# Kernel tuning notes

Measured on AMD Instinct MI355X. Metric: run time of the kernel, lower is better.

The kernel has to match this reference:

```python
import jax, jax.numpy as jnp
import numpy as np

B, L, D = 16, 1024, 768

def setup_inputs() -> dict:
    key = jax.random.key(0)
    ks = jax.random.split(key, 6)
    s = 1.0 / np.sqrt(D)  # torch Linear default init scale
    return {
        "h": jax.random.normal(ks[0], (B, L, D), dtype=jnp.float32),
        "q": jax.random.normal(ks[1], (B, L, D), dtype=jnp.float32),
        "w1_w": jax.random.uniform(ks[2], (L, D), jnp.float32, -s, s),
        "w1_b": jax.random.uniform(ks[3], (L,), jnp.float32, -s, s),
        "w2_w": jax.random.uniform(ks[4], (L, D), jnp.float32, -s, s),
        "w2_b": jax.random.uniform(ks[5], (L,), jnp.float32, -s, s),
    }

def reference(h, q, w1_w, w1_b, w2_w, w2_b):
    # w1h: [B, L, l], w2q: [B, L, l] -> permuted [B, l, L]
    w1h = jnp.einsum('bsd,ld->bsl', h, w1_w) + w1_b
    w2q = jnp.einsum('btd,ld->btl', q, w2_w) + w2_b
    w3hq = jnp.einsum('bsd,btd->bst', h, q)           # [B, L, L]
    a = w1h + jnp.swapaxes(w2q, 1, 2) + w3hq          # [B, L, L]
    p = jax.nn.softmax(a, axis=2)
    c = jnp.einsum('bst,btd->bsd', p, q)              # [B, L, D]
    m = jnp.max(a, axis=2)                            # [B, L]
    p2 = jax.nn.softmax(m, axis=1)                    # [B, L]
    qc = h * p2[:, :, None]                           # [B, L, D]
    return jnp.concatenate([h, c, h * c, qc * c], axis=2)  # [B, L, 4D]
```

## Files before the change

### kernel.cpp

```cpp
#include <hip/hip_runtime.h>
#include <stdint.h>

#define B_  16
#define L_  1024
#define D_  768
#define K1_ 1536

typedef unsigned short u16;
typedef __attribute__((ext_vector_type(4))) float f32x4;
typedef __attribute__((ext_vector_type(8))) _Float16 f16x8;

__device__ __forceinline__ u16 f2h(float x){
    return __builtin_bit_cast(u16, (_Float16)x);
}

__device__ __forceinline__ void gload_lds16(const void* g, void* l){
    __builtin_amdgcn_global_load_lds((const __attribute__((address_space(1))) void*)g,
                                     (__attribute__((address_space(3))) void*)l, 16, 0, 0);
}

__global__ __launch_bounds__(256) void prep(const float* __restrict__ h, const float* __restrict__ q,
    const float* __restrict__ w1w, const float* __restrict__ w2w,
    u16* __restrict__ hH, u16* __restrict__ wH, u16* __restrict__ qH,
    u16* __restrict__ w1h, u16* __restrict__ qT, int b0, int nb)
{
    __shared__ float tile[32][33];
    int bb = blockIdx.z, bg = b0 + bb;
    int t0 = blockIdx.x * 32, d0 = blockIdx.y * 32;
    int tid = threadIdx.x;
    int r  = tid >> 3;
    int c4 = (tid & 7) * 4;
    int t = t0 + r, d = d0 + c4;
    size_t goff = (size_t)t * D_ + d;

    float4 qv  = *(const float4*)(q   + (size_t)bg * L_ * D_ + goff);
    float4 hv  = *(const float4*)(h   + (size_t)bg * L_ * D_ + goff);
    float4 w2v = *(const float4*)(w2w + goff);

    tile[r][c4 + 0] = qv.x; tile[r][c4 + 1] = qv.y;
    tile[r][c4 + 2] = qv.z; tile[r][c4 + 3] = qv.w;

    size_t o = ((size_t)bb * L_ + t) * D_ + d;
    ushort4 a;
    a.x = f2h(hv.x); a.y = f2h(hv.y); a.z = f2h(hv.z); a.w = f2h(hv.w);
    *(ushort4*)(hH + o) = a;
    a.x = f2h(hv.x + w2v.x); a.y = f2h(hv.y + w2v.y);
    a.z = f2h(hv.z + w2v.z); a.w = f2h(hv.w + w2v.w);
    *(ushort4*)(wH + o) = a;
    a.x = f2h(qv.x); a.y = f2h(qv.y); a.z = f2h(qv.z); a.w = f2h(qv.w);
    *(ushort4*)(qH + o) = a;
    if (bb == 0){
        float4 w1v = *(const float4*)(w1w + goff);
        a.x = f2h(w1v.x); a.y = f2h(w1v.y); a.z = f2h(w1v.z); a.w = f2h(w1v.w);
        *(ushort4*)(w1h + goff) = a;
    }
    __syncthreads();
    int dr = tid >> 3;
    int tc = (tid & 7) * 4;
    ushort4 b;
    b.x = f2h(tile[tc + 0][dr]); b.y = f2h(tile[tc + 1][dr]);
    b.z = f2h(tile[tc + 2][dr]); b.w = f2h(tile[tc + 3][dr]);
    *(ushort4*)(qT + (size_t)bb * D_ * L_ + (size_t)(d0 + dr) * L_ + t0 + tc) = b;
}

__global__ __launch_bounds__(512) void gemm1(
    const u16* __restrict__ hH, const u16* __restrict__ wH,
    const u16* __restrict__ qH, const u16* __restrict__ w1h,
    const float* __restrict__ w1b, const float* __restrict__ w2b,
    u16* __restrict__ pT, float* __restrict__ mT, float* __restrict__ sT)
{
    __shared__ u16 ldsA[2][256 * 64];
    __shared__ u16 ldsB[2][256 * 64];
    int nwg = gridDim.x;
    int o = blockIdx.x;
    int wg = (o & 7) * (nwg >> 3) + (o >> 3);
    int bb = wg >> 4;
    int tl = wg & 15;
    int smb = tl >> 2, tnb = tl & 3;
    int s0 = smb * 256, t0 = tnb * 256;
    int tid = threadIdx.x;
    int lane = tid & 63, wid = tid >> 6;
    int wm2 = wid >> 2, wn2 = wid & 3;
    int l15 = lane & 15, l4 = lane >> 4;

    const u16* hHb = hH + (size_t)bb * L_ * D_;
    const u16* wHb = wH + (size_t)bb * L_ * D_;
    const u16* qHb = qH + (size_t)bb * L_ * D_;

    f32x4 acc[8][4];
    #pragma unroll
    for (int m = 0; m < 8; m++)
        #pragma unroll
        for (int n = 0; n < 4; n++)
            acc[m][n] = (f32x4){0.f, 0.f, 0.f, 0.f};

    auto stage = [&](int t){
        int kb = t * 64;
        bool inH = (kb < D_);
        const u16* As = inH ? hHb : wHb;
        const u16* Bs = inH ? w1h : qHb;
        int koff = inH ? kb : (kb - D_);
        int buf = t & 1;
        #pragma unroll
        for (int q = 0; q < 4; q++){
            int idx = q * 512 + tid;
            int row = idx >> 3, c = idx & 7;
            int cc = c ^ (row & 7);
            int dst = (q * 512 + wid * 64) * 8;
            gload_lds16(As + (size_t)(s0 + row) * D_ + koff + cc * 8, &ldsA[buf][dst]);
            gload_lds16(Bs + (size_t)(t0 + row) * D_ + koff + cc * 8, &ldsB[buf][dst]);
        }
    };

    stage(0);
    asm volatile("s_waitcnt vmcnt(0)" ::: "memory");
    __builtin_amdgcn_s_barrier();

    for (int t = 0; t < 24; t++){
        if (t + 1 < 24) stage(t + 1);
        int bsel = t & 1;
        #pragma unroll
        for (int kk = 0; kk < 2; kk++){
            f16x8 bf[4];
            #pragma unroll
            for (int n = 0; n < 4; n++){
                int row = wn2 * 64 + n * 16 + l15;
                int c = kk * 4 + l4;
                bf[n] = *(const f16x8*)&ldsB[bsel][(row * 8 + (c ^ (row & 7))) * 8];
            }
            #pragma unroll
            for (int mh = 0; mh < 2; mh++){
                f16x8 af[4];
                #pragma unroll
                for (int mi = 0; mi < 4; mi++){
                    int row = wm2 * 128 + (mh * 4 + mi) * 16 + l15;
                    int c = kk * 4 + l4;
                    af[mi] = *(const f16x8*)&ldsA[bsel][(row * 8 + (c ^ (row & 7))) * 8];
                }
                __builtin_amdgcn_s_setprio(1);
                #pragma unroll
                for (int mi = 0; mi < 4; mi++)
                    #pragma unroll
                    for (int n = 0; n < 4; n++)
                        acc[mh * 4 + mi][n] = __builtin_amdgcn_mfma_f32_16x16x32_f16(
                            af[mi], bf[n], acc[mh * 4 + mi][n], 0, 0, 0);
                __builtin_amdgcn_s_setprio(0);
            }
        }
        asm volatile("s_waitcnt vmcnt(0)" ::: "memory");
        __builtin_amdgcn_s_barrier();
    }

    u16* pRow = pT + (size_t)bb * L_ * L_;
    #pragma unroll
    for (int m = 0; m < 8; m++){
        #pragma unroll
        for (int r = 0; r < 4; r++){
            int s = s0 + wm2 * 128 + m * 16 + l4 * 4 + r;
            float w2v = w2b[s];
            float v[4];
            float tmax = -1e30f;
            #pragma unroll
            for (int n = 0; n < 4; n++){
                int tcol = t0 + wn2 * 64 + n * 16 + l15;
                v[n] = acc[m][n][r] + w1b[tcol] + w2v;
                tmax = fmaxf(tmax, v[n]);
            }
            #pragma unroll
            for (int o2 = 1; o2 < 16; o2 <<= 1)
                tmax = fmaxf(tmax, __shfl_xor(tmax, o2));
            float e[4];
            float gsum = 0.f;
            #pragma unroll
            for (int n = 0; n < 4; n++){
                e[n] = __expf(v[n] - tmax);
                gsum += e[n];
            }
            #pragma unroll
            for (int n = 0; n < 4; n++){
                int tcol = t0 + wn2 * 64 + n * 16 + l15;
                pRow[(size_t)s * L_ + tcol] = f2h(e[n]);
            }
            #pragma unroll
            for (int o2 = 1; o2 < 16; o2 <<= 1)
                gsum += __shfl_xor(gsum, o2);
            if (l15 == 0){
                size_t mo = ((size_t)bb * L_ + s) * 16 + tnb * 4 + wn2;
                mT[mo] = tmax;
                sT[mo] = gsum;
            }
        }
    }
}

__global__ __launch_bounds__(1024) void p2k(const float* __restrict__ mT, const float* __restrict__ sT,
                                            float* __restrict__ p2, float* __restrict__ sc, int b0)
{
    __shared__ float red[16];
    int bb = blockIdx.x, bg = b0 + bb;
    int tid = threadIdx.x;
    const float4* mv = (const float4*)(mT + ((size_t)bb * L_ + tid) * 16);
    float4 m0 = mv[0], m1 = mv[1], m2 = mv[2], m3 = mv[3];
    float mj[16] = {m0.x, m0.y, m0.z, m0.w, m1.x, m1.y, m1.z, m1.w,
                    m2.x, m2.y, m2.z, m2.w, m3.x, m3.y, m3.z, m3.w};
    float v = mj[0];
    #pragma unroll
    for (int i = 1; i < 16; i++) v = fmaxf(v, mj[i]);

    float mx = v;
    #pragma unroll
    for (int o = 32; o; o >>= 1) mx = fmaxf(mx, __shfl_xor(mx, o));
    if ((tid & 63) == 0) red[tid >> 6] = mx;
    __syncthreads();
    float m2g = red[0];
    #pragma unroll
    for (int i = 1; i < 16; i++) m2g = fmaxf(m2g, red[i]);
    float e = __expf(v - m2g);
    float sum = e;
    #pragma unroll
    for (int o = 32; o; o >>= 1) sum += __shfl_xor(sum, o);
    __syncthreads();
    if ((tid & 63) == 0) red[tid >> 6] = sum;
    __syncthreads();
    float st = 0.f;
    #pragma unroll
    for (int i = 0; i < 16; i++) st += red[i];
    p2[(size_t)bg * L_ + tid] = e / st;

    const float4* sv = (const float4*)(sT + ((size_t)bb * L_ + tid) * 16);
    float4 s0v = sv[0], s1v = sv[1], s2v = sv[2], s3v = sv[3];
    float sj[16] = {s0v.x, s0v.y, s0v.z, s0v.w, s1v.x, s1v.y, s1v.z, s1v.w,
                    s2v.x, s2v.y, s2v.z, s2v.w, s3v.x, s3v.y, s3v.z, s3v.w};
    float ej[16];
    float S = 0.f;
    #pragma unroll
    for (int j = 0; j < 16; j++){
        ej[j] = __expf(mj[j] - v);
        S += sj[j] * ej[j];
    }
    float invS = 1.0f / S;
    float* scb = sc + (size_t)bb * 16 * L_;
    #pragma unroll
    for (int j = 0; j < 16; j++)
        scb[j * L_ + tid] = ej[j] * invS;
}

__global__ __launch_bounds__(512) void gemm2(const u16* __restrict__ pT, const u16* __restrict__ qT,
    const float* __restrict__ sc, float* __restrict__ out, int b0)
{
    __shared__ u16 ldsA[2][256 * 64];
    __shared__ u16 ldsB[2][256 * 64];
    int nwg = gridDim.x;
    int o = blockIdx.x;
    int wg = ((nwg & 7) == 0) ? ((o & 7) * (nwg >> 3) + (o >> 3)) : o;
    int bb = wg / 12;
    int tl = wg % 12;
    int smb = tl >> 2, dnb = tl & 3;
    smb = tl / 3; dnb = tl % 3;
    int s0 = smb * 256, d0 = dnb * 256;
    int tid = threadIdx.x;
    int lane = tid & 63, wid = tid >> 6;
    int wm2 = wid >> 2, wn2 = wid & 3;
    int l15 = lane & 15, l4 = lane >> 4;

    const u16* Ab = pT + (size_t)bb * L_ * L_;
    const u16* Bb = qT + (size_t)bb * D_ * L_;
    const float* scb = sc + (size_t)bb * 16 * L_;

    f32x4 acc[8][4];
    #pragma unroll
    for (int m = 0; m < 8; m++)
        #pragma unroll
        for (int n = 0; n < 4; n++)
            acc[m][n] = (f32x4){0.f, 0.f, 0.f, 0.f};

    auto stage = [&](int t){
        int kb = t * 64;
        int buf = t & 1;
        #pragma unroll
        for (int q = 0; q < 4; q++){
            int idx = q * 512 + tid;
            int row = idx >> 3, c = idx & 7;
            int cc = c ^ (row & 7);
            int dst = (q * 512 + wid * 64) * 8;
            gload_lds16(Ab + (size_t)(s0 + row) * L_ + kb + cc * 8, &ldsA[buf][dst]);
            gload_lds16(Bb + (size_t)(d0 + row) * L_ + kb + cc * 8, &ldsB[buf][dst]);
        }
    };

    stage(0);
    asm volatile("s_waitcnt vmcnt(0)" ::: "memory");
    __builtin_amdgcn_s_barrier();

    for (int t = 0; t < 16; t++){
        if (t + 1 < 16) stage(t + 1);
        int bsel = t & 1;
        _Float16 sch[8];
        #pragma unroll
        for (int m = 0; m < 8; m++)
            sch[m] = (_Float16)scb[(size_t)t * L_ + s0 + wm2 * 128 + m * 16 + l15];
        #pragma unroll
        for (int kk = 0; kk < 2; kk++){
            f16x8 bf[4];
            #pragma unroll
            for (int n = 0; n < 4; n++){
                int row = wn2 * 64 + n * 16 + l15;
                int c = kk * 4 + l4;
                bf[n] = *(const f16x8*)&ldsB[bsel][(row * 8 + (c ^ (row & 7))) * 8];
            }
            #pragma unroll
            for (int mh = 0; mh < 2; mh++){
                f16x8 af[4];
                #pragma unroll
                for (int mi = 0; mi < 4; mi++){
                    int row = wm2 * 128 + (mh * 4 + mi) * 16 + l15;
                    int c = kk * 4 + l4;
                    af[mi] = *(const f16x8*)&ldsA[bsel][(row * 8 + (c ^ (row & 7))) * 8];
                    af[mi] = af[mi] * sch[mh * 4 + mi];
                }
                __builtin_amdgcn_s_setprio(1);
                #pragma unroll
                for (int mi = 0; mi < 4; mi++)
                    #pragma unroll
                    for (int n = 0; n < 4; n++)
                        acc[mh * 4 + mi][n] = __builtin_amdgcn_mfma_f32_16x16x32_f16(
                            af[mi], bf[n], acc[mh * 4 + mi][n], 0, 0, 0);
                __builtin_amdgcn_s_setprio(0);
            }
        }
        asm volatile("s_waitcnt vmcnt(0)" ::: "memory");
        __builtin_amdgcn_s_barrier();
    }

    float* oC = out + ((size_t)(b0 + bb) * L_) * (4 * D_) + D_;
    #pragma unroll
    for (int m = 0; m < 8; m++){
        int sbase = s0 + wm2 * 128 + m * 16 + l4 * 4;
        #pragma unroll
        for (int r = 0; r < 4; r++){
            int s = sbase + r;
            #pragma unroll
            for (int n = 0; n < 4; n++){
                int d = d0 + wn2 * 64 + n * 16 + l15;
                oC[(size_t)s * (4 * D_) + d] = acc[m][n][r];
            }
        }
    }
}

__global__ __launch_bounds__(192) void epi(const float* __restrict__ h,
    const float* __restrict__ p2, float* __restrict__ out, int b0)
{
    int rowid = blockIdx.x;
    int bb = rowid >> 10, s = rowid & 1023;
    int bg = b0 + bb;
    float p2v = p2[(size_t)bg * L_ + s];
    const float* hR = h + ((size_t)bg * L_ + s) * D_;
    float* oR = out + ((size_t)bg * L_ + s) * (4 * D_);
    int d = threadIdx.x * 4;
    float4 cv = *(const float4*)(oR + D_ + d);
    float4 hv = *(const float4*)(hR + d);
    float4 hc = {hv.x * cv.x, hv.y * cv.y, hv.z * cv.z, hv.w * cv.w};
    float4 qc = {p2v * hc.x, p2v * hc.y, p2v * hc.z, p2v * hc.w};
    *(float4*)(oR + d)          = hv;
    *(float4*)(oR + 2 * D_ + d) = hc;
    *(float4*)(oR + 3 * D_ + d) = qc;
}

extern "C" void kernel_launch(void* const* d_in, const int* in_sizes, int n_in,
                              void* d_out, int out_size, void* d_ws, size_t ws_size,
                              hipStream_t stream)
{
    const float* h   = (const float*)d_in[0];
    const float* q   = (const float*)d_in[1];
    const float* w1w = (const float*)d_in[2];
    const float* w1b = (const float*)d_in[3];
    const float* w2w = (const float*)d_in[4];
    const float* w2b = (const float*)d_in[5];
    float* out = (float*)d_out;

    const size_t szPlane = (size_t)L_ * D_ * 2;
    const size_t szM     = (size_t)B_ * L_ * 4;
    const size_t perB_pT = (size_t)L_ * L_ * 2;
    const size_t perB_s  = (size_t)L_ * 16 * 4;
    const size_t perB = 4 * szPlane + perB_pT + 3 * perB_s;
    const size_t fixed = szPlane + szM;

    int NB = 1;
    if (ws_size > fixed){
        size_t nbc = (ws_size - fixed) / perB;
        NB = (nbc >= 16) ? 16 : (nbc < 1 ? 1 : (int)nbc);
    }

    char* p = (char*)d_ws;
    u16*   w1h  = (u16*)p;   p += szPlane;
    float* p2   = (float*)p; p += szM;
    float* mT   = (float*)p; p += perB_s * NB;
    float* sT   = (float*)p; p += perB_s * NB;
    float* sc   = (float*)p; p += perB_s * NB;
    u16*   hH   = (u16*)p;   p += szPlane * NB;
    u16*   wH   = (u16*)p;   p += szPlane * NB;
    u16*   qH   = (u16*)p;   p += szPlane * NB;
    u16*   qT   = (u16*)p;   p += szPlane * NB;
    u16*   pT   = (u16*)p;

    for (int b0 = 0; b0 < B_; b0 += NB){
        int nb = (B_ - b0 < NB) ? (B_ - b0) : NB;
        prep  <<<dim3(32, 24, nb), 256, 0, stream>>>(h, q, w1w, w2w, hH, wH, qH, w1h, qT, b0, nb);
        gemm1 <<<dim3(16 * nb), 512, 0, stream>>>(hH, wH, qH, w1h, w1b, w2b, pT, mT, sT);
        p2k   <<<dim3(nb), 1024, 0, stream>>>(mT, sT, p2, sc, b0);
        gemm2 <<<dim3(12 * nb), 512, 0, stream>>>(pT, qT, sc, out, b0);
        epi   <<<dim3(nb * 1024), 192, 0, stream>>>(h, p2, out, b0);
    }
}
```

Before: 202.7 us.

## Retile gemm2 to 256x192 tiles and read fp16 h in epilogue

gemm2's output tiles shrink from 256x256 to 256x192, giving 16 workgroups per batch instead of 12. This is meant to fill the GPU more evenly, at the cost of less B-operand reuse per tile. The epilogue now reads the fp16 copy of h made in prep instead of the fp32 input, halving that read traffic. The h, h*c and qc output columns therefore carry fp16 rounding of h, which loses precision compared to copying the fp32 input.

```diff
diff --git a/kernel.cpp b/kernel.cpp
--- a/kernel.cpp
+++ b/kernel.cpp
@@ -12,6 +12,9 @@
 
 __device__ __forceinline__ u16 f2h(float x){
     return __builtin_bit_cast(u16, (_Float16)x);
+}
+__device__ __forceinline__ float h2f(u16 x){
+    return (float)__builtin_bit_cast(_Float16, x);
 }
 
 __device__ __forceinline__ void gload_lds16(const void* g, void* l){
@@ -249,15 +252,14 @@
     const float* __restrict__ sc, float* __restrict__ out, int b0)
 {
     __shared__ u16 ldsA[2][256 * 64];
-    __shared__ u16 ldsB[2][256 * 64];
+    __shared__ u16 ldsB[2][192 * 64];
     int nwg = gridDim.x;
     int o = blockIdx.x;
     int wg = ((nwg & 7) == 0) ? ((o & 7) * (nwg >> 3) + (o >> 3)) : o;
-    int bb = wg / 12;
-    int tl = wg % 12;
+    int bb = wg >> 4;
+    int tl = wg & 15;
     int smb = tl >> 2, dnb = tl & 3;
-    smb = tl / 3; dnb = tl % 3;
-    int s0 = smb * 256, d0 = dnb * 256;
+    int s0 = smb * 256, d0 = dnb * 192;
     int tid = threadIdx.x;
     int lane = tid & 63, wid = tid >> 6;
     int wm2 = wid >> 2, wn2 = wid & 3;
@@ -267,24 +269,31 @@
     const u16* Bb = qT + (size_t)bb * D_ * L_;
     const float* scb = sc + (size_t)bb * 16 * L_;
 
-    f32x4 acc[8][4];
+    f32x4 acc[8][3];
     #pragma unroll
     for (int m = 0; m < 8; m++)
         #pragma unroll
-        for (int n = 0; n < 4; n++)
+        for (int n = 0; n < 3; n++)
             acc[m][n] = (f32x4){0.f, 0.f, 0.f, 0.f};
 
     auto stage = [&](int t){
         int kb = t * 64;
         int buf = t & 1;
         #pragma unroll
-        for (int q = 0; q < 4; q++){
-            int idx = q * 512 + tid;
+        for (int qq = 0; qq < 4; qq++){
+            int idx = qq * 512 + tid;
             int row = idx >> 3, c = idx & 7;
             int cc = c ^ (row & 7);
-            int dst = (q * 512 + wid * 64) * 8;
-            gload_lds16(Ab + (size_t)(s0 + row) * L_ + kb + cc * 8, &ldsA[buf][dst]);
-            gload_lds16(Bb + (size_t)(d0 + row) * L_ + kb + cc * 8, &ldsB[buf][dst]);
+            gload_lds16(Ab + (size_t)(s0 + row) * L_ + kb + cc * 8,
+                        &ldsA[buf][(qq * 512 + wid * 64) * 8]);
+        }
+        #pragma unroll
+        for (int qq = 0; qq < 3; qq++){
+            int idx = qq * 512 + tid;
+            int row = idx >> 3, c = idx & 7;
+            int cc = c ^ (row & 7);
+            gload_lds16(Bb + (size_t)(d0 + row) * L_ + kb + cc * 8,
+                        &ldsB[buf][(qq * 512 + wid * 64) * 8]);
         }
     };
 
@@ -301,10 +310,10 @@
             sch[m] = (_Float16)scb[(size_t)t * L_ + s0 + wm2 * 128 + m * 16 + l15];
         #pragma unroll
         for (int kk = 0; kk < 2; kk++){
-            f16x8 bf[4];
-            #pragma unroll
-            for (int n = 0; n < 4; n++){
-                int row = wn2 * 64 + n * 16 + l15;
+            f16x8 bf[3];
+            #pragma unroll
+            for (int n = 0; n < 3; n++){
+                int row = wn2 * 48 + n * 16 + l15;
                 int c = kk * 4 + l4;
                 bf[n] = *(const f16x8*)&ldsB[bsel][(row * 8 + (c ^ (row & 7))) * 8];
             }
@@ -322,7 +331,7 @@
                 #pragma unroll
                 for (int mi = 0; mi < 4; mi++)
                     #pragma unroll
-                    for (int n = 0; n < 4; n++)
+                    for (int n = 0; n < 3; n++)
                         acc[mh * 4 + mi][n] = __builtin_amdgcn_mfma_f32_16x16x32_f16(
                             af[mi], bf[n], acc[mh * 4 + mi][n], 0, 0, 0);
                 __builtin_amdgcn_s_setprio(0);
@@ -340,26 +349,27 @@
         for (int r = 0; r < 4; r++){
             int s = sbase + r;
             #pragma unroll
-            for (int n = 0; n < 4; n++){
-                int d = d0 + wn2 * 64 + n * 16 + l15;
+            for (int n = 0; n < 3; n++){
+                int d = d0 + wn2 * 48 + n * 16 + l15;
                 oC[(size_t)s * (4 * D_) + d] = acc[m][n][r];
             }
         }
     }
 }
 
-__global__ __launch_bounds__(192) void epi(const float* __restrict__ h,
+__global__ __launch_bounds__(192) void epi(const u16* __restrict__ hH,
     const float* __restrict__ p2, float* __restrict__ out, int b0)
 {
     int rowid = blockIdx.x;
     int bb = rowid >> 10, s = rowid & 1023;
     int bg = b0 + bb;
     float p2v = p2[(size_t)bg * L_ + s];
-    const float* hR = h + ((size_t)bg * L_ + s) * D_;
+    const u16* hR = hH + ((size_t)bb * L_ + s) * D_;
     float* oR = out + ((size_t)bg * L_ + s) * (4 * D_);
     int d = threadIdx.x * 4;
     float4 cv = *(const float4*)(oR + D_ + d);
-    float4 hv = *(const float4*)(hR + d);
+    ushort4 hu = *(const ushort4*)(hR + d);
+    float4 hv = {h2f(hu.x), h2f(hu.y), h2f(hu.z), h2f(hu.w)};
     float4 hc = {hv.x * cv.x, hv.y * cv.y, hv.z * cv.z, hv.w * cv.w};
     float4 qc = {p2v * hc.x, p2v * hc.y, p2v * hc.z, p2v * hc.w};
     *(float4*)(oR + d)          = hv;
@@ -409,7 +419,7 @@
         prep  <<<dim3(32, 24, nb), 256, 0, stream>>>(h, q, w1w, w2w, hH, wH, qH, w1h, qT, b0, nb);
         gemm1 <<<dim3(16 * nb), 512, 0, stream>>>(hH, wH, qH, w1h, w1b, w2b, pT, mT, sT);
         p2k   <<<dim3(nb), 1024, 0, stream>>>(mT, sT, p2, sc, b0);
-        gemm2 <<<dim3(12 * nb), 512, 0, stream>>>(pT, qT, sc, out, b0);
-        epi   <<<dim3(nb * 1024), 192, 0, stream>>>(h, p2, out, b0);
-    }
-}
+        gemm2 <<<dim3(16 * nb), 512, 0, stream>>>(pT, qT, sc, out, b0);
+        epi   <<<dim3(nb * 1024), 192, 0, stream>>>(hH, p2, out, b0);
+    }
+}
```

Result: faster. 193.9 us (median of 2 runs) (-4.3%).
